# Kernel optimization log

Hardware: AMD Instinct MI355X
Metric: run time of the kernel (lower is better)

The kernel has to match this reference:

```python
import jax, jax.numpy as jnp
import numpy as np

K = 3        # kernel_size
PAD = 1      # padding ('same' for stride 1)
RANK = 53    # CP rank from compression=10: round(27*32*64/(10*(9+32+64)))


def _kaiming_uniform(key, shape, fan_in):
    # matches nn.init.kaiming_uniform_(a=sqrt(5)): bound = 1/sqrt(fan_in)
    bound = 1.0 / np.sqrt(fan_in)
    return jax.random.uniform(key, shape, jnp.float32, -bound, bound)


def setup_inputs() -> dict:
    key = jax.random.key(0)
    ks = jax.random.split(key, 7)
    B, Cin, Cout, H, W, D = 1, 32, 64, 56, 56, 56
    x = jax.random.normal(ks[0], (B, Cin, H, W, D), jnp.float32)
    # CP factor matrices (fan_in = second dim for torch's 2D kaiming)
    U_kh = _kaiming_uniform(ks[1], (K, RANK), RANK)
    U_kw = _kaiming_uniform(ks[2], (K, RANK), RANK)
    U_kd = _kaiming_uniform(ks[3], (K, RANK), RANK)
    U_cin = _kaiming_uniform(ks[4], (Cin, RANK), RANK)
    U_cout = _kaiming_uniform(ks[5], (RANK, Cout), Cout)
    bias = jax.random.normal(ks[6], (Cout,), jnp.float32)
    return {"x": x, "U_kh": U_kh, "U_kw": U_kw, "U_kd": U_kd,
            "U_cin": U_cin, "U_cout": U_cout, "bias": bias}


def reference(x, U_kh, U_kw, U_kd, U_cin, U_cout, bias):
    B, C, H, W, D = x.shape
    xp = jnp.pad(x, ((0, 0), (0, 0), (PAD, PAD), (PAD, PAD), (PAD, PAD)))
    # im2col patches: patches[i,j,l,b,c,x,y,z] = xp[b,c,x+i,y+j,z+l]
    # (same values/ordering as torch unfold(2).unfold(3).unfold(4), stride=1)
    patches = jnp.stack([
        xp[:, :, i:i + H, j:j + W, l:l + D]
        for i in range(K) for j in range(K) for l in range(K)
    ]).reshape(K, K, K, B, C, H, W, D)
    # CP tensor-network contraction (legs: k_h,k_w,k_d,c_in share rank r -> c_out)
    out = jnp.einsum('ijlbcxyz,ir,jr,lr,cr,ro->boxyz',
                     patches, U_kh, U_kw, U_kd, U_cin, U_cout,
                     optimize=True)
    return out + bias[None, :, None, None, None]
```

## Files before the change

kernel.cpp:

```cpp
#include <hip/hip_runtime.h>


#define NP 175616
#define NP2 87808
#define HSTR 3136
#define H2 1568
#define W2 28
#define CIN 32
#define RK 53
#define RC0 27
#define COUT 64
#define SCR 53

__global__ __launch_bounds__(256) void k0_t(const float* __restrict__ Ucin,
                                            float* __restrict__ Ut)
{
    int t = blockIdx.x * 256 + threadIdx.x;
    if (t < RK * CIN) {
        int r = t >> 5, c = t & 31;
        Ut[t] = Ucin[c * RK + r];
    }
}

__global__ __launch_bounds__(256, 8) void k1d(
    const float* __restrict__ x, const float* __restrict__ Ut,
    const float* __restrict__ Ukd, float* __restrict__ T1d)
{
    const int lane = threadIdx.x & 63;
    const int row  = blockIdx.x * 4 + (threadIdx.x >> 6);
    const int p    = row * 56 + lane;
    const bool act = (lane < 56);
    const int pc   = act ? p : (p - 8);

    float xv[CIN];
#pragma unroll
    for (int c = 0; c < CIN; ++c) xv[c] = x[c * NP + pc];
#pragma unroll
    for (int c = 0; c < CIN; ++c) asm volatile("" : "+v"(xv[c]));

    const int r0 = blockIdx.y * 6;
    const int nr = (r0 + 6 <= RK) ? 6 : (RK - r0);

    float acc[6];
#pragma unroll
    for (int rr = 0; rr < 6; ++rr) {
        if (rr < nr) {
            const float* U = Ut + (r0 + rr) * CIN;
            float a0 = 0.f, a1 = 0.f, a2 = 0.f, a3 = 0.f;
#pragma unroll
            for (int c = 0; c < CIN; c += 4) {
                a0 += xv[c]     * U[c];
                a1 += xv[c + 1] * U[c + 1];
                a2 += xv[c + 2] * U[c + 2];
                a3 += xv[c + 3] * U[c + 3];
            }
            acc[rr] = (a0 + a1) + (a2 + a3);
        }
    }

    float lm[6], rp[6];
#pragma unroll
    for (int rr = 0; rr < 6; ++rr) {
        if (rr < nr) {
            lm[rr] = __shfl_up(acc[rr], 1, 64);
            rp[rr] = __shfl_down(acc[rr], 1, 64);
        }
    }

#pragma unroll
    for (int rr = 0; rr < 6; ++rr) {
        if (rr < nr) {
            const int r = r0 + rr;
            float l  = (lane == 0)  ? 0.f : lm[rr];
            float rv = (lane == 55) ? 0.f : rp[rr];
            float res = l * Ukd[r] + acc[rr] * Ukd[RK + r] + rv * Ukd[2 * RK + r];
            if (act) T1d[(size_t)r * NP + p] = res;
        }
    }
}

__global__ __launch_bounds__(512, 4) void k3c(
    const float2* __restrict__ Ta, const float* __restrict__ Ucout,
    const float* __restrict__ bias, const float* __restrict__ Ukh,
    const float* __restrict__ Ukw, float2* __restrict__ Out)
{
    __shared__ float2 tld[RC0][64];

    const int lane = threadIdx.x & 63;
    const int wv   = threadIdx.x >> 6;

    const int nwg = gridDim.x;
    const int qx = nwg >> 3, rx = nwg & 7;
    const int xcd = blockIdx.x & 7, loc = blockIdx.x >> 3;
    const int swz = ((xcd < rx) ? xcd * (qx + 1) : rx * (qx + 1) + (xcd - rx) * qx) + loc;

    const int q  = swz * 64 + lane;
    const int h  = q / H2;
    const int rm = q - h * H2;
    const int w  = rm / W2;
    const int om = (h > 0)  ? -H2 : 0;
    const int op = (h < 55) ?  H2 : 0;
    const int oa = (w > 0)  ? -W2 : 0;
    const int oc = (w < 55) ?  W2 : 0;
    const float mh0 = (h > 0)  ? 1.f : 0.f;
    const float mh2 = (h < 55) ? 1.f : 0.f;
    const float mw0 = (w > 0)  ? 1.f : 0.f;
    const float mw2 = (w < 55) ? 1.f : 0.f;

    const float2* Sq = Ta + q;
    const int og = __builtin_amdgcn_readfirstlane(wv << 3);

    float2 a[8];

#pragma unroll 1
    for (int r = wv; r < RC0; r += 8) {
        const float2* S = Sq + (size_t)r * NP2;
        const float kw0 = mw0 * Ukw[r];
        const float kw1 = Ukw[RK + r];
        const float kw2 = mw2 * Ukw[2 * RK + r];
        const float kh0 = mh0 * Ukh[r];
        const float kh1 = Ukh[RK + r];
        const float kh2 = mh2 * Ukh[2 * RK + r];
        float2 v00 = S[om + oa], v01 = S[om], v02 = S[om + oc];
        float2 v10 = S[oa],      v11 = S[0],  v12 = S[oc];
        float2 v20 = S[op + oa], v21 = S[op], v22 = S[op + oc];
        float2 t;
        t.x = (v00.x * kw0 + v01.x * kw1 + v02.x * kw2) * kh0
            + (v10.x * kw0 + v11.x * kw1 + v12.x * kw2) * kh1
            + (v20.x * kw0 + v21.x * kw1 + v22.x * kw2) * kh2;
        t.y = (v00.y * kw0 + v01.y * kw1 + v02.y * kw2) * kh0
            + (v10.y * kw0 + v11.y * kw1 + v12.y * kw2) * kh1
            + (v20.y * kw0 + v21.y * kw1 + v22.y * kw2) * kh2;
        tld[r][lane] = t;
    }
    __syncthreads();

#pragma unroll
    for (int o = 0; o < 8; ++o) {
        float b = bias[og + o];
        a[o].x = b; a[o].y = b;
    }
#pragma unroll 4
    for (int r = 0; r < RC0; ++r) {
        float2 t = tld[r][lane];
        const float* Ur = Ucout + r * COUT + og;
#pragma unroll
        for (int o = 0; o < 8; ++o) {
            float u = Ur[o];
            a[o].x += t.x * u; a[o].y += t.y * u;
        }
    }
    __syncthreads();

#pragma unroll 1
    for (int r = RC0 + wv; r < RK; r += 8) {
        const float2* S = Sq + (size_t)r * NP2;
        const float kw0 = mw0 * Ukw[r];
        const float kw1 = Ukw[RK + r];
        const float kw2 = mw2 * Ukw[2 * RK + r];
        const float kh0 = mh0 * Ukh[r];
        const float kh1 = Ukh[RK + r];
        const float kh2 = mh2 * Ukh[2 * RK + r];
        float2 v00 = S[om + oa], v01 = S[om], v02 = S[om + oc];
        float2 v10 = S[oa],      v11 = S[0],  v12 = S[oc];
        float2 v20 = S[op + oa], v21 = S[op], v22 = S[op + oc];
        float2 t;
        t.x = (v00.x * kw0 + v01.x * kw1 + v02.x * kw2) * kh0
            + (v10.x * kw0 + v11.x * kw1 + v12.x * kw2) * kh1
            + (v20.x * kw0 + v21.x * kw1 + v22.x * kw2) * kh2;
        t.y = (v00.y * kw0 + v01.y * kw1 + v02.y * kw2) * kh0
            + (v10.y * kw0 + v11.y * kw1 + v12.y * kw2) * kh1
            + (v20.y * kw0 + v21.y * kw1 + v22.y * kw2) * kh2;
        tld[r - RC0][lane] = t;
    }
    __syncthreads();

#pragma unroll 4
    for (int r = RC0; r < RK; ++r) {
        float2 t = tld[r - RC0][lane];
        const float* Ur = Ucout + r * COUT + og;
#pragma unroll
        for (int o = 0; o < 8; ++o) {
            float u = Ur[o];
            a[o].x += t.x * u; a[o].y += t.y * u;
        }
    }

#pragma unroll
    for (int o = 0; o < 8; ++o)
        Out[(size_t)(og + o) * NP2 + q] = a[o];
}


__global__ __launch_bounds__(256) void k1_chunk(
    const float* __restrict__ x, const float* __restrict__ Ucin,
    float* T, int r0, int nr)
{
    __shared__ float sU[11 * CIN];
    const int tid = threadIdx.x;
    for (int t = tid; t < nr * CIN; t += 256) {
        int lr = t >> 5, c = t & 31;
        sU[t] = Ucin[c * RK + (r0 + lr)];
    }
    __syncthreads();
    const int p = blockIdx.x * 256 + tid;
    float xv[CIN];
#pragma unroll
    for (int c = 0; c < CIN; ++c) xv[c] = x[c * NP + p];
#pragma unroll 1
    for (int lr = 0; lr < nr; ++lr) {
        float acc = 0.f;
#pragma unroll
        for (int c = 0; c < CIN; ++c) acc += xv[c] * sU[lr * CIN + c];
        T[(size_t)(SCR + lr) * NP + p] = acc;
    }
}

__global__ __launch_bounds__(256) void k2_chunk(
    const float* __restrict__ Ukh, const float* __restrict__ Ukw,
    const float* __restrict__ Ukd, float* T, int r0)
{
    __shared__ float sIn[5800];
    __shared__ float sA[5600];
    const int lr = blockIdx.z;
    const int r  = r0 + lr;
    const int h0 = blockIdx.x * 8, w0 = blockIdx.y * 8;
    const int tid = threadIdx.x;
    const float kh0 = Ukh[r], kh1 = Ukh[RK + r], kh2 = Ukh[2 * RK + r];
    const float kw0 = Ukw[r], kw1 = Ukw[RK + r], kw2 = Ukw[2 * RK + r];
    const float kd0 = Ukd[r], kd1 = Ukd[RK + r], kd2 = Ukd[2 * RK + r];
    const float* T1r = T + (size_t)(SCR + lr) * NP;

    for (int idx = tid; idx < 5800; idx += 256) {
        int d = idx % 58; int t2 = idx / 58; int ww = t2 % 10; int hh = t2 / 10;
        int gh = h0 + hh - 1, gw = w0 + ww - 1, gd = d - 1;
        float v = 0.f;
        if ((unsigned)gh < 56u && (unsigned)gw < 56u && (unsigned)gd < 56u)
            v = T1r[gh * HSTR + gw * 56 + gd];
        sIn[idx] = v;
    }
    __syncthreads();
    for (int idx = tid; idx < 5600; idx += 256) {
        int d = idx % 56; int t2 = idx / 56; int ww = t2 % 10; int hh = t2 / 10;
        const float* b = &sIn[(hh * 10 + ww) * 58 + d];
        sA[idx] = b[0] * kd0 + b[1] * kd1 + b[2] * kd2;
    }
    __syncthreads();
    const float k00 = kh0 * kw0, k01 = kh0 * kw1, k02 = kh0 * kw2;
    const float k10 = kh1 * kw0, k11 = kh1 * kw1, k12 = kh1 * kw2;
    const float k20 = kh2 * kw0, k21 = kh2 * kw1, k22 = kh2 * kw2;
    for (int idx = tid; idx < 3584; idx += 256) {
        int d = idx % 56; int t2 = idx / 56; int ww = t2 % 8; int hh = t2 / 8;
        const float* a = &sA[(hh * 10 + ww) * 56 + d];
        float acc = a[0]    * k00 + a[56]   * k01 + a[112]  * k02
                  + a[560]  * k10 + a[616]  * k11 + a[672]  * k12
                  + a[1120] * k20 + a[1176] * k21 + a[1232] * k22;
        T[(size_t)r * NP + (h0 + hh) * HSTR + (w0 + ww) * 56 + d] = acc;
    }
}

__global__ __launch_bounds__(256) void k3_out(
    float* T, const float* __restrict__ Ucout, const float* __restrict__ bias)
{
    __shared__ float sUo[RK * COUT];
    __shared__ float sB[COUT];
    const int tid = threadIdx.x;
    for (int t = tid; t < RK * COUT; t += 256) sUo[t] = Ucout[t];
    if (tid < COUT) sB[tid] = bias[tid];
    __syncthreads();
    const int p = blockIdx.x * 256 + tid;
    float acc[COUT];
#pragma unroll
    for (int o = 0; o < COUT; ++o) acc[o] = sB[o];
#pragma unroll 1
    for (int r = 0; r < RK; ++r) {
        float t = T[(size_t)r * NP + p];
        const float* Ur = &sUo[r * COUT];
#pragma unroll
        for (int o = 0; o < COUT; ++o) acc[o] += t * Ur[o];
    }
#pragma unroll
    for (int o = 0; o < COUT; ++o) T[(size_t)o * NP + p] = acc[o];
}


extern "C" void kernel_launch(void* const* d_in, const int* in_sizes, int n_in,
                              void* d_out, int out_size, void* d_ws, size_t ws_size,
                              hipStream_t stream)
{
    const float* x     = (const float*)d_in[0];
    const float* Ukh   = (const float*)d_in[1];
    const float* Ukw   = (const float*)d_in[2];
    const float* Ukd   = (const float*)d_in[3];
    const float* Ucin  = (const float*)d_in[4];
    const float* Ucout = (const float*)d_in[5];
    const float* bias  = (const float*)d_in[6];

    const size_t t1_bytes = (size_t)RK * NP * sizeof(float);

    if (ws_size >= t1_bytes + 8192) {
        float* T1 = (float*)d_ws;
        float* Ut = (float*)((char*)d_ws + t1_bytes);
        k0_t<<<7, 256, 0, stream>>>(Ucin, Ut);
        k1d<<<dim3(HSTR / 4, 9), 256, 0, stream>>>(x, Ut, Ukd, T1);
        k3c<<<NP2 / 64, 512, 0, stream>>>((const float2*)T1, Ucout, bias, Ukh,
                                          Ukw, (float2*)d_out);
    } else {
        float* T = (float*)d_out;
        for (int r0 = 0; r0 < RK; r0 += 11) {
            int nr = (RK - r0 < 11) ? (RK - r0) : 11;
            k1_chunk<<<NP / 256, 256, 0, stream>>>(x, Ucin, T, r0, nr);
            k2_chunk<<<dim3(7, 7, nr), 256, 0, stream>>>(Ukh, Ukw, Ukd, T, r0);
        }
        k3_out<<<NP / 256, 256, 0, stream>>>(T, Ucout, bias);
    }
}
```

Before: 143.5 us.

## Cut k1d rank groups to four and split k3 output channels across two blocks

k1d now runs 4 rank groups of about 13 ranks each, processed in inner batches of 5, instead of 9 groups of 6. This cuts how often x is reloaded per rank group. k3c becomes k3z with 256-thread blocks and twice as many blocks. Each block handles half of the 64 output channels (selected by z), and 4 waves now stride over ranks. The price is that both halves recompute the 3x3 stencil over T1, roughly doubling k3's T1 reads.

Result: slower. 174.9 us (+21.9%).

```diff
diff --git a/kernel.cpp b/kernel.cpp
--- a/kernel.cpp
+++ b/kernel.cpp
@@ -38,48 +38,49 @@
 #pragma unroll
     for (int c = 0; c < CIN; ++c) asm volatile("" : "+v"(xv[c]));
 
-    const int r0 = blockIdx.y * 6;
-    const int nr = (r0 + 6 <= RK) ? 6 : (RK - r0);
-
-    float acc[6];
-#pragma unroll
-    for (int rr = 0; rr < 6; ++rr) {
-        if (rr < nr) {
-            const float* U = Ut + (r0 + rr) * CIN;
-            float a0 = 0.f, a1 = 0.f, a2 = 0.f, a3 = 0.f;
-#pragma unroll
-            for (int c = 0; c < CIN; c += 4) {
-                a0 += xv[c]     * U[c];
-                a1 += xv[c + 1] * U[c + 1];
-                a2 += xv[c + 2] * U[c + 2];
-                a3 += xv[c + 3] * U[c + 3];
+    const int r0 = blockIdx.y * 13;
+    const int r1 = (blockIdx.y == 3) ? RK : (r0 + 13);
+
+#pragma unroll 1
+    for (int rs = r0; rs < r1; rs += 5) {
+        const int nb = (r1 - rs < 5) ? (r1 - rs) : 5;
+        float acc[5], lm[5], rp[5];
+#pragma unroll
+        for (int j = 0; j < 5; ++j) {
+            if (j < nb) {
+                const float* U = Ut + (rs + j) * CIN;
+                float a0 = 0.f, a1 = 0.f, a2 = 0.f, a3 = 0.f;
+#pragma unroll
+                for (int c = 0; c < CIN; c += 4) {
+                    a0 += xv[c]     * U[c];
+                    a1 += xv[c + 1] * U[c + 1];
+                    a2 += xv[c + 2] * U[c + 2];
+                    a3 += xv[c + 3] * U[c + 3];
+                }
+                acc[j] = (a0 + a1) + (a2 + a3);
             }
-            acc[rr] = (a0 + a1) + (a2 + a3);
-        }
-    }
-
-    float lm[6], rp[6];
-#pragma unroll
-    for (int rr = 0; rr < 6; ++rr) {
-        if (rr < nr) {
-            lm[rr] = __shfl_up(acc[rr], 1, 64);
-            rp[rr] = __shfl_down(acc[rr], 1, 64);
-        }
-    }
-
-#pragma unroll
-    for (int rr = 0; rr < 6; ++rr) {
-        if (rr < nr) {
-            const int r = r0 + rr;
-            float l  = (lane == 0)  ? 0.f : lm[rr];
-            float rv = (lane == 55) ? 0.f : rp[rr];
-            float res = l * Ukd[r] + acc[rr] * Ukd[RK + r] + rv * Ukd[2 * RK + r];
-            if (act) T1d[(size_t)r * NP + p] = res;
-        }
-    }
-}
-
-__global__ __launch_bounds__(512, 4) void k3c(
+        }
+#pragma unroll
+        for (int j = 0; j < 5; ++j) {
+            if (j < nb) {
+                lm[j] = __shfl_up(acc[j], 1, 64);
+                rp[j] = __shfl_down(acc[j], 1, 64);
+            }
+        }
+#pragma unroll
+        for (int j = 0; j < 5; ++j) {
+            if (j < nb) {
+                const int r = rs + j;
+                float l  = (lane == 0)  ? 0.f : lm[j];
+                float rv = (lane == 55) ? 0.f : rp[j];
+                float res = l * Ukd[r] + acc[j] * Ukd[RK + r] + rv * Ukd[2 * RK + r];
+                if (act) T1d[(size_t)r * NP + p] = res;
+            }
+        }
+    }
+}
+
+__global__ __launch_bounds__(256, 8) void k3z(
     const float2* __restrict__ Ta, const float* __restrict__ Ucout,
     const float* __restrict__ bias, const float* __restrict__ Ukh,
     const float* __restrict__ Ukw, float2* __restrict__ Out)
@@ -94,7 +95,10 @@
     const int xcd = blockIdx.x & 7, loc = blockIdx.x >> 3;
     const int swz = ((xcd < rx) ? xcd * (qx + 1) : rx * (qx + 1) + (xcd - rx) * qx) + loc;
 
-    const int q  = swz * 64 + lane;
+    const int bx = swz >> 1;
+    const int z  = swz & 1;
+
+    const int q  = bx * 64 + lane;
     const int h  = q / H2;
     const int rm = q - h * H2;
     const int w  = rm / W2;
@@ -108,12 +112,12 @@
     const float mw2 = (w < 55) ? 1.f : 0.f;
 
     const float2* Sq = Ta + q;
-    const int og = __builtin_amdgcn_readfirstlane(wv << 3);
+    const int og = __builtin_amdgcn_readfirstlane(z * 32 + (wv << 3));
 
     float2 a[8];
 
 #pragma unroll 1
-    for (int r = wv; r < RC0; r += 8) {
+    for (int r = wv; r < RC0; r += 4) {
         const float2* S = Sq + (size_t)r * NP2;
         const float kw0 = mw0 * Ukw[r];
         const float kw1 = Ukw[RK + r];
@@ -153,7 +157,7 @@
     __syncthreads();
 
 #pragma unroll 1
-    for (int r = RC0 + wv; r < RK; r += 8) {
+    for (int r = RC0 + wv; r < RK; r += 4) {
         const float2* S = Sq + (size_t)r * NP2;
         const float kw0 = mw0 * Ukw[r];
         const float kw1 = Ukw[RK + r];
@@ -302,8 +306,8 @@
         float* T1 = (float*)d_ws;
         float* Ut = (float*)((char*)d_ws + t1_bytes);
         k0_t<<<7, 256, 0, stream>>>(Ucin, Ut);
-        k1d<<<dim3(HSTR / 4, 9), 256, 0, stream>>>(x, Ut, Ukd, T1);
-        k3c<<<NP2 / 64, 512, 0, stream>>>((const float2*)T1, Ucout, bias, Ukh,
+        k1d<<<dim3(HSTR / 4, 4), 256, 0, stream>>>(x, Ut, Ukd, T1);
+        k3z<<<NP2 / 32, 256, 0, stream>>>((const float2*)T1, Ucout, bias, Ukh,
                                           Ukw, (float2*)d_out);
     } else {
         float* T = (float*)d_out;
```
